# Kernel optimization log

Measured on AMD Instinct MI355X. Metric: run time of the kernel, lower is better.

Reference implementation:

```python
import jax, jax.numpy as jnp
import numpy as np

EMBED = 1024
HEADS = 16
HEAD_DIM = EMBED // HEADS
HIDDEN = 4096
EPS = 1e-5


def setup_inputs() -> dict:
    key = jax.random.key(0)
    ks = jax.random.split(key, 16)
    s_e = 1.0 / np.sqrt(EMBED)
    s_h = 1.0 / np.sqrt(HIDDEN)
    return {
        "x": jax.random.normal(ks[0], (8, 1024, EMBED), dtype=jnp.float32),
        "ln1_g": jnp.ones((EMBED,), jnp.float32),
        "ln1_b": jnp.zeros((EMBED,), jnp.float32),
        "ln2_g": jnp.ones((EMBED,), jnp.float32),
        "ln2_b": jnp.zeros((EMBED,), jnp.float32),
        "wq": jax.random.uniform(ks[1], (EMBED, EMBED), jnp.float32, -s_e, s_e),
        "bq": jax.random.uniform(ks[2], (EMBED,), jnp.float32, -s_e, s_e),
        "wk": jax.random.uniform(ks[3], (EMBED, EMBED), jnp.float32, -s_e, s_e),
        "bk": jax.random.uniform(ks[4], (EMBED,), jnp.float32, -s_e, s_e),
        "wv": jax.random.uniform(ks[5], (EMBED, EMBED), jnp.float32, -s_e, s_e),
        "bv": jax.random.uniform(ks[6], (EMBED,), jnp.float32, -s_e, s_e),
        "wo": jax.random.uniform(ks[7], (EMBED, EMBED), jnp.float32, -s_e, s_e),
        "bo": jax.random.uniform(ks[8], (EMBED,), jnp.float32, -s_e, s_e),
        "w1": jax.random.uniform(ks[9], (EMBED, HIDDEN), jnp.float32, -s_e, s_e),
        "b1": jax.random.uniform(ks[10], (HIDDEN,), jnp.float32, -s_e, s_e),
        "w2": jax.random.uniform(ks[11], (HIDDEN, EMBED), jnp.float32, -s_h, s_h),
        "b2": jax.random.uniform(ks[12], (EMBED,), jnp.float32, -s_h, s_h),
    }


def _layernorm(x, g, b):
    mu = jnp.mean(x, axis=-1, keepdims=True)
    var = jnp.mean((x - mu) ** 2, axis=-1, keepdims=True)
    return (x - mu) * jax.lax.rsqrt(var + EPS) * g + b


def reference(x, ln1_g, ln1_b, ln2_g, ln2_b, wq, bq, wk, bk, wv, bv, wo, bo, w1, b1, w2, b2):
    B, N, E = x.shape
    scale = HEAD_DIM ** (-0.5)
    # --- attention sublayer (pre-norm) ---
    h = _layernorm(x, ln1_g, ln1_b)
    q = (h @ wq + bq).reshape(B, N, HEADS, HEAD_DIM).transpose(0, 2, 1, 3) * scale
    k = (h @ wk + bk).reshape(B, N, HEADS, HEAD_DIM).transpose(0, 2, 1, 3)
    v = (h @ wv + bv).reshape(B, N, HEADS, HEAD_DIM).transpose(0, 2, 1, 3)
    scores = jnp.einsum("bhqd,bhkd->bhqk", q, k)
    attn = jax.nn.softmax(scores, axis=-1)
    ctx = jnp.einsum("bhqk,bhkd->bhqd", attn, v)
    ctx = ctx.transpose(0, 2, 1, 3).reshape(B, N, E)
    x = x + (ctx @ wo + bo)
    # --- FFN sublayer (pre-norm) ---
    h2 = _layernorm(x, ln2_g, ln2_b)
    ff = jax.nn.relu(h2 @ w1 + b1) @ w2 + b2
    return x + ff
```

## Files before the change

### kernel.cpp

```cpp
#include <hip/hip_runtime.h>
#include <hip/hip_bf16.h>

typedef __attribute__((ext_vector_type(4))) float f32x4;
typedef __attribute__((ext_vector_type(16))) float f32x16;
typedef __attribute__((ext_vector_type(8))) __bf16 bf16x8;
typedef __attribute__((ext_vector_type(4))) __bf16 bf16x4;
typedef __attribute__((ext_vector_type(4))) unsigned int u32x4;

static constexpr int E    = 1024;
static constexpr int TOK  = 8192;
static constexpr int HID  = 4096;

#define DEVINL __device__ __forceinline__

DEVINL void gload16(const void* g, void* l) {
  __builtin_amdgcn_global_load_lds((__attribute__((address_space(1))) void*)g,
                                   (__attribute__((address_space(3))) void*)l, 16, 0, 0);
}

#define ABAR()  asm volatile("s_barrier" ::: "memory")
#define AVM(n)  asm volatile("s_waitcnt vmcnt(" #n ")" ::: "memory")
#define CVTPK(dst, lo, hi) asm("v_cvt_pk_bf16_f32 %0, %1, %2" : "=v"(dst) : "v"(lo), "v"(hi))
#define PLSWAP(a, b) asm("v_permlane32_swap_b32 %0, %1" : "+v"(a), "+v"(b))

template <int N> DEVINL void avm() {
  if constexpr (N == 0)      asm volatile("s_waitcnt vmcnt(0)" ::: "memory");
  else if constexpr (N == 2) asm volatile("s_waitcnt vmcnt(2)" ::: "memory");
  else if constexpr (N == 8) asm volatile("s_waitcnt vmcnt(8)" ::: "memory");
  else if constexpr (N == 9) asm volatile("s_waitcnt vmcnt(9)" ::: "memory");
  else                       asm volatile("s_waitcnt vmcnt(0)" ::: "memory");
}

__global__ __launch_bounds__(256) void wconv_kernel(const float* __restrict__ W,
                                                    __bf16* __restrict__ Wt,
                                                    int K, int N) {
  __shared__ float tile[32][33];
  const int t  = threadIdx.x;
  const long k0 = (long)blockIdx.y * 32;
  const long n0 = (long)blockIdx.x * 32;
  const int r  = t >> 3;
  const int c4 = (t & 7) * 4;
  float4 v = *(const float4*)&W[(k0 + r) * N + n0 + c4];
  tile[r][c4 + 0] = v.x; tile[r][c4 + 1] = v.y;
  tile[r][c4 + 2] = v.z; tile[r][c4 + 3] = v.w;
  __syncthreads();
  bf16x4 o;
#pragma unroll
  for (int i = 0; i < 4; ++i) o[i] = (__bf16)tile[c4 + i][r];
  *(bf16x4*)&Wt[(n0 + r) * K + k0 + c4] = o;
}

__global__ __launch_bounds__(256) void ln_kernel(const float* __restrict__ X,
                                                 const float* __restrict__ g,
                                                 const float* __restrict__ be,
                                                 __bf16* __restrict__ O) {
  const int t = threadIdx.x;
  const long row = blockIdx.x;
  float4 v = *(const float4*)&X[row * E + t * 4];
  float s  = v.x + v.y + v.z + v.w;
  float ss = v.x * v.x + v.y * v.y + v.z * v.z + v.w * v.w;
#pragma unroll
  for (int off = 32; off; off >>= 1) {
    s  += __shfl_down(s, off);
    ss += __shfl_down(ss, off);
  }
  __shared__ float red[8];
  const int w = t >> 6;
  if ((t & 63) == 0) { red[w] = s; red[4 + w] = ss; }
  __syncthreads();
  s  = red[0] + red[1] + red[2] + red[3];
  ss = red[4] + red[5] + red[6] + red[7];
  const float mean = s * (1.0f / E);
  const float var  = ss * (1.0f / E) - mean * mean;
  const float rstd = rsqrtf(var + 1e-5f);
  float4 gv = *(const float4*)&g[t * 4];
  float4 bv = *(const float4*)&be[t * 4];
  bf16x4 o;
  o[0] = (__bf16)((v.x - mean) * rstd * gv.x + bv.x);
  o[1] = (__bf16)((v.y - mean) * rstd * gv.y + bv.y);
  o[2] = (__bf16)((v.z - mean) * rstd * gv.z + bv.z);
  o[3] = (__bf16)((v.w - mean) * rstd * gv.w + bv.w);
  *(bf16x4*)&O[row * E + t * 4] = o;
}

template <int BM_, int DEPTH, bool RELU, bool RESID, bool OUTBF, int NB>
__global__ __launch_bounds__(512, 2) void gemmk_kernel(const __bf16* __restrict__ A,
                                                       const __bf16* __restrict__ Bt,
                                                       const float* __restrict__ bias0,
                                                       const float* __restrict__ bias1,
                                                       const float* __restrict__ bias2,
                                                       const float* resid,
                                                       void* Cout,
                                                       int M, int N, int K) {
  extern __shared__ char lds[];
  constexpr int MF    = BM_ / 32;
  constexpr int ABYT  = BM_ * 64;
  constexpr int TILEB = ABYT + 16384;
  constexpr int AL    = BM_ / 128;
  constexpr int TL    = AL + 2;
  constexpr int W     = (DEPTH - 2) * TL;

  const int tid  = threadIdx.x;
  const int lane = tid & 63;
  const int l15  = lane & 15;
  const int kp   = lane >> 4;
  const int wid  = tid >> 6;
  const int wr   = wid >> 2;
  const int wc   = wid & 3;

  const int nwg  = gridDim.x * gridDim.y;
  const int flat = blockIdx.x + gridDim.x * blockIdx.y;
  const int swz  = (flat & 7) * (nwg >> 3) + (flat >> 3);
  const int bx   = swz % gridDim.x;
  const int by   = swz / gridDim.x;
  const long brow = (long)by * BM_;
  const long bcol = (long)bx * 256;

  const __bf16* Ab = A  + brow * K;
  const __bf16* Bb = Bt + bcol * K;
  const int NT = K >> 5;

  auto stageA = [&](int k0, char* dst) {
#pragma unroll
    for (int i = 0; i < AL; ++i) {
      const int c = i * 512 + tid;
      const int r = c >> 2;
      const int p = (c & 3) ^ ((r >> 1) & 3);
      gload16(Ab + (long)r * K + k0 + p * 8, dst + c * 16);
    }
  };
  auto stageB = [&](int k0, char* dst) {
#pragma unroll
    for (int i = 0; i < 2; ++i) {
      const int c = i * 512 + tid;
      const int r = c >> 2;
      const int p = (c & 3) ^ ((r >> 1) & 3);
      gload16(Bb + (long)r * K + k0 + p * 8, dst + c * 16);
    }
  };

  f32x4 acc[MF][4];
  const f32x4 z4 = {0.f, 0.f, 0.f, 0.f};
#pragma unroll
  for (int m = 0; m < MF; ++m)
#pragma unroll
    for (int n = 0; n < 4; ++n) acc[m][n] = z4;

#pragma unroll
  for (int pt = 0; pt < DEPTH - 1; ++pt) {
    stageA(pt * 32, lds + pt * TILEB);
    stageB(pt * 32, lds + pt * TILEB + ABYT);
  }

  bf16x8 af[MF > 4 ? 4 : MF], bfr[4];

  for (int t = 0; t < NT; ++t) {
    const int cb = t % DEPTH;
    const int sb = (t + DEPTH - 1) % DEPTH;
    const char* Ac = lds + cb * TILEB;
    const char* Bc = Ac + ABYT;
    char* An = lds + sb * TILEB;
    const int kt = (t + DEPTH - 1 < NT) ? ((t + DEPTH - 1) << 5) : 0;

    avm<W>();
    ABAR();

    if constexpr (BM_ == 256) {
#pragma unroll
      for (int m = 0; m < 4; ++m) {
        const int row = m * 32 + wr * 16 + l15;
        af[m] = *(const bf16x8*)(Ac + row * 64 + (kp ^ ((row >> 1) & 3)) * 16);
      }
#pragma unroll
      for (int n = 0; n < 4; ++n) {
        const int col = n * 64 + wc * 16 + l15;
        bfr[n] = *(const bf16x8*)(Bc + col * 64 + (kp ^ ((col >> 1) & 3)) * 16);
      }
      stageA(kt, An);
      __builtin_amdgcn_s_setprio(1);
#pragma unroll
      for (int m = 0; m < 4; ++m)
#pragma unroll
        for (int n = 0; n < 4; ++n)
          acc[m][n] = __builtin_amdgcn_mfma_f32_16x16x32_bf16(af[m], bfr[n], acc[m][n], 0, 0, 0);
      __builtin_amdgcn_s_setprio(0);
#pragma unroll
      for (int m = 0; m < 4; ++m) {
        const int row = (m + 4) * 32 + wr * 16 + l15;
        af[m] = *(const bf16x8*)(Ac + row * 64 + (kp ^ ((row >> 1) & 3)) * 16);
      }
      stageB(kt, An + ABYT);
      __builtin_amdgcn_s_setprio(1);
#pragma unroll
      for (int m = 0; m < 4; ++m)
#pragma unroll
        for (int n = 0; n < 4; ++n)
          acc[m + 4][n] = __builtin_amdgcn_mfma_f32_16x16x32_bf16(af[m], bfr[n], acc[m + 4][n], 0, 0, 0);
      __builtin_amdgcn_s_setprio(0);
    } else {
#pragma unroll
      for (int m = 0; m < 4; ++m) {
        const int row = m * 32 + wr * 16 + l15;
        af[m] = *(const bf16x8*)(Ac + row * 64 + (kp ^ ((row >> 1) & 3)) * 16);
      }
#pragma unroll
      for (int n = 0; n < 4; ++n) {
        const int col = n * 64 + wc * 16 + l15;
        bfr[n] = *(const bf16x8*)(Bc + col * 64 + (kp ^ ((col >> 1) & 3)) * 16);
      }
      stageA(kt, An);
      stageB(kt, An + ABYT);
      __builtin_amdgcn_s_setprio(1);
#pragma unroll
      for (int m = 0; m < 4; ++m)
#pragma unroll
        for (int n = 0; n < 4; ++n)
          acc[m][n] = __builtin_amdgcn_mfma_f32_16x16x32_bf16(af[m], bfr[n], acc[m][n], 0, 0, 0);
      __builtin_amdgcn_s_setprio(0);
    }
  }
  avm<0>();

#pragma unroll
  for (int m = 0; m < MF; ++m) {
#pragma unroll
    for (int n = 0; n < 4; ++n) {
      const long col = bcol + n * 64 + wc * 16 + l15;
      float bb;
      if (NB == 3) {
        const float* bp = (col < 1024) ? bias0 : ((col < 2048) ? bias1 : bias2);
        bb = bp[col & 1023];
      } else {
        bb = bias0[col];
      }
#pragma unroll
      for (int j = 0; j < 4; ++j) {
        const long row = brow + m * 32 + wr * 16 + (lane >> 4) * 4 + j;
        float val = acc[m][n][j] + bb;
        if (RELU) val = fmaxf(val, 0.f);
        const long idx = row * N + col;
        if (RESID) val += resid[idx];
        if (OUTBF) ((__bf16*)Cout)[idx] = (__bf16)val;
        else       ((float*)Cout)[idx]  = val;
      }
    }
  }
}

__global__ __launch_bounds__(256, 3) void attn_kernel(const __bf16* __restrict__ QKV,
                                                      __bf16* __restrict__ Og) {
  __shared__ __align__(16) __bf16 Qs[128 * 64];
  __shared__ __align__(16) __bf16 Ks[2][64 * 64];
  __shared__ __align__(16) __bf16 Vt[2][64 * 64];

  const int QSTR = 3072;
  const int t    = threadIdx.x;
  const int lane = t & 63;
  const int w    = t >> 6;
  const int l31  = lane & 31;
  const int h    = lane >> 5;
  const int b    = blockIdx.y >> 4;
  const int hh   = blockIdx.y & 15;
  const long row0 = (long)b * 1024 + (long)blockIdx.x * 128;
  const long kvrow0 = (long)b * 1024;
  const int colQ = hh * 64;
  const int colK = colQ + 1024;
  const int colV = colQ + 2048;

#pragma unroll
  for (int j = 0; j < 4; ++j) {
    const int c = j * 256 + t;
    const int r = c >> 3;
    const int p = (c & 7) ^ (r & 7);
    gload16(QKV + (row0 + r) * QSTR + colQ + p * 8, (char*)Qs + c * 16);
  }
#pragma unroll
  for (int j = 0; j < 2; ++j) {
    const int c = j * 256 + t;
    const int r = c >> 3;
    const int p = (c & 7) ^ (r & 7);
    gload16(QKV + (kvrow0 + r) * QSTR + colK + p * 8, (char*)Ks[0] + c * 16);
  }
  bf16x8 vv[2];
#pragma unroll
  for (int j = 0; j < 2; ++j) {
    const int c = j * 256 + t;
    const int key = c >> 3, dc = c & 7;
    vv[j] = *(const bf16x8*)(QKV + (kvrow0 + key) * QSTR + colV + dc * 8);
  }
  AVM(0);
#pragma unroll
  for (int j = 0; j < 2; ++j) {
    const int c = j * 256 + t;
    const int key = c >> 3, dc = c & 7;
#pragma unroll
    for (int e = 0; e < 8; ++e) {
      const int d = dc * 8 + e;
      *(__bf16*)((char*)Vt[0] + d * 128 + (((key >> 3) ^ dc) * 16) + (key & 7) * 2) = vv[j][e];
    }
  }
  __syncthreads();

  bf16x8 bq[4];
  {
    const int qrow = w * 32 + l31;
#pragma unroll
    for (int kk = 0; kk < 4; ++kk) {
      const int p = (kk * 2 + h) ^ (qrow & 7);
      bq[kk] = *(const bf16x8*)((const char*)Qs + qrow * 128 + p * 16);
    }
  }

  f32x16 ctx0, ctx1;
#pragma unroll
  for (int r = 0; r < 16; ++r) { ctx0[r] = 0.f; ctx1[r] = 0.f; }
  float m = -INFINITY, l = 0.f;

  for (int kb = 0; kb < 16; ++kb) {
    const int cur = kb & 1, nxt = cur ^ 1;
    const int kb1 = (kb + 1 < 16) ? kb + 1 : kb;
    const long kr1 = kvrow0 + kb1 * 64;

#pragma unroll
    for (int j = 0; j < 2; ++j) {
      const int c = j * 256 + t;
      const int key = c >> 3, dc = c & 7;
      vv[j] = *(const bf16x8*)(QKV + (kr1 + key) * QSTR + colV + dc * 8);
    }
#pragma unroll
    for (int j = 0; j < 2; ++j) {
      const int c = j * 256 + t;
      const int r = c >> 3;
      const int p = (c & 7) ^ (r & 7);
      gload16(QKV + (kr1 + r) * QSTR + colK + p * 8, (char*)Ks[nxt] + c * 16);
    }

    f32x16 s0, s1;
#pragma unroll
    for (int r = 0; r < 16; ++r) { s0[r] = 0.f; s1[r] = 0.f; }
    __builtin_amdgcn_s_setprio(1);
#pragma unroll
    for (int kk = 0; kk < 4; ++kk) {
      const int pce = kk * 2 + h;
      const int p0i = pce ^ (l31 & 7);
      bf16x8 ak0 = *(const bf16x8*)((const char*)Ks[cur] + l31 * 128 + p0i * 16);
      bf16x8 ak1 = *(const bf16x8*)((const char*)Ks[cur] + (32 + l31) * 128 + p0i * 16);
      s0 = __builtin_amdgcn_mfma_f32_32x32x16_bf16(ak0, bq[kk], s0, 0, 0, 0);
      s1 = __builtin_amdgcn_mfma_f32_32x32x16_bf16(ak1, bq[kk], s1, 0, 0, 0);
    }
    __builtin_amdgcn_s_setprio(0);

    float mx = s0[0];
#pragma unroll
    for (int r = 1; r < 16; ++r) mx = fmaxf(mx, s0[r]);
#pragma unroll
    for (int r = 0; r < 16; ++r) mx = fmaxf(mx, s1[r]);
    mx = fmaxf(mx, __shfl_xor(mx, 32));

    if (!__all(mx - m <= 64.f)) {
      const float mn = fmaxf(m, mx);
      const float corr = __expf((m - mn) * 0.125f);
      l *= corr;
#pragma unroll
      for (int r = 0; r < 16; ++r) { ctx0[r] *= corr; ctx1[r] *= corr; }
      m = mn;
    }
    f32x16 p0, p1;
    float rs = 0.f;
#pragma unroll
    for (int r = 0; r < 16; ++r) { p0[r] = __expf((s0[r] - m) * 0.125f); rs += p0[r]; }
#pragma unroll
    for (int r = 0; r < 16; ++r) { p1[r] = __expf((s1[r] - m) * 0.125f); rs += p1[r]; }
    rs += __shfl_xor(rs, 32);
    l += rs;

    AVM(2);
#pragma unroll
    for (int j = 0; j < 2; ++j) {
      const int c = j * 256 + t;
      const int key = c >> 3, dc = c & 7;
#pragma unroll
      for (int e = 0; e < 8; ++e) {
        const int d = dc * 8 + e;
        *(__bf16*)((char*)Vt[nxt] + d * 128 + (((key >> 3) ^ dc) * 16) + (key & 7) * 2) = vv[j][e];
      }
    }

    bf16x8 paf[4];
#pragma unroll
    for (int ks = 0; ks < 4; ++ks) {
      const int base = (ks & 1) * 8;
      unsigned a0, a1, b0, b1;
      if (ks < 2) {
        CVTPK(a0, p0[base + 0], p0[base + 1]);
        CVTPK(b0, p0[base + 4], p0[base + 5]);
        CVTPK(a1, p0[base + 2], p0[base + 3]);
        CVTPK(b1, p0[base + 6], p0[base + 7]);
      } else {
        CVTPK(a0, p1[base + 0], p1[base + 1]);
        CVTPK(b0, p1[base + 4], p1[base + 5]);
        CVTPK(a1, p1[base + 2], p1[base + 3]);
        CVTPK(b1, p1[base + 6], p1[base + 7]);
      }
      PLSWAP(a0, b0);
      PLSWAP(a1, b1);
      u32x4 wv4; wv4[0] = a0; wv4[1] = a1; wv4[2] = b0; wv4[3] = b1;
      paf[ks] = __builtin_bit_cast(bf16x8, wv4);
    }

    __builtin_amdgcn_s_setprio(1);
#pragma unroll
    for (int ks = 0; ks < 4; ++ks) {
      const int pce = ks * 2 + h;
      bf16x8 av0 = *(const bf16x8*)((const char*)Vt[cur] + l31 * 128 + ((pce ^ (l31 >> 3)) * 16));
      bf16x8 av1 = *(const bf16x8*)((const char*)Vt[cur] + (32 + l31) * 128 + ((pce ^ (4 + (l31 >> 3))) * 16));
      ctx0 = __builtin_amdgcn_mfma_f32_32x32x16_bf16(av0, paf[ks], ctx0, 0, 0, 0);
      ctx1 = __builtin_amdgcn_mfma_f32_32x32x16_bf16(av1, paf[ks], ctx1, 0, 0, 0);
    }
    __builtin_amdgcn_s_setprio(0);

    __syncthreads();
  }

  const float inv = 1.0f / l;
  const long orow = row0 + w * 32 + l31;
#pragma unroll
  for (int f = 0; f < 2; ++f)
#pragma unroll
    for (int tq = 0; tq < 4; ++tq) {
      bf16x4 o;
#pragma unroll
      for (int e = 0; e < 4; ++e) {
        const float v = (f ? ctx1[tq * 4 + e] : ctx0[tq * 4 + e]) * inv;
        o[e] = (__bf16)v;
      }
      const int col = colQ + f * 32 + tq * 8 + h * 4;
      *(bf16x4*)&Og[orow * E + col] = o;
    }
}

extern "C" void kernel_launch(void* const* d_in, const int* in_sizes, int n_in,
                              void* d_out, int out_size, void* d_ws, size_t ws_size,
                              hipStream_t stream) {
  const float* x     = (const float*)d_in[0];
  const float* ln1g  = (const float*)d_in[1];
  const float* ln1b  = (const float*)d_in[2];
  const float* ln2g  = (const float*)d_in[3];
  const float* ln2b  = (const float*)d_in[4];
  const float* wq    = (const float*)d_in[5];
  const float* bq    = (const float*)d_in[6];
  const float* wk    = (const float*)d_in[7];
  const float* bk    = (const float*)d_in[8];
  const float* wv    = (const float*)d_in[9];
  const float* bv    = (const float*)d_in[10];
  const float* wo    = (const float*)d_in[11];
  const float* bo    = (const float*)d_in[12];
  const float* w1    = (const float*)d_in[13];
  const float* b1    = (const float*)d_in[14];
  const float* w2    = (const float*)d_in[15];
  const float* b2    = (const float*)d_in[16];
  float* out = (float*)d_out;

  char* ws = (char*)d_ws;
  const size_t MB = 1024 * 1024;
  __bf16* Wqkv = (__bf16*)(ws + 0 * MB);
  __bf16* Wot  = (__bf16*)(ws + 6 * MB);
  __bf16* W1t  = (__bf16*)(ws + 8 * MB);
  __bf16* W2t  = (__bf16*)(ws + 16 * MB);
  __bf16* h    = (__bf16*)(ws + 24 * MB);
  __bf16* qkv  = (__bf16*)(ws + 40 * MB);
  __bf16* ctx  = (__bf16*)(ws + 88 * MB);
  __bf16* ff1  = (__bf16*)(ws + 40 * MB);

  const dim3 blk(256);
  const dim3 blk512(512);
  const size_t GLDS256 = 4 * (256 * 64 + 16384);
  const size_t GLDS128 = 5 * (128 * 64 + 16384);

  wconv_kernel<<<dim3(E / 32, E / 32), blk, 0, stream>>>(wq, Wqkv, E, E);
  wconv_kernel<<<dim3(E / 32, E / 32), blk, 0, stream>>>(wk, Wqkv + 1024 * 1024, E, E);
  wconv_kernel<<<dim3(E / 32, E / 32), blk, 0, stream>>>(wv, Wqkv + 2048 * 1024, E, E);
  wconv_kernel<<<dim3(E / 32, E / 32), blk, 0, stream>>>(wo, Wot, E, E);
  wconv_kernel<<<dim3(HID / 32, E / 32), blk, 0, stream>>>(w1, W1t, E, HID);
  wconv_kernel<<<dim3(E / 32, HID / 32), blk, 0, stream>>>(w2, W2t, HID, E);

  ln_kernel<<<TOK, blk, 0, stream>>>(x, ln1g, ln1b, h);

  gemmk_kernel<256, 4, false, false, true, 3><<<dim3(3072 / 256, TOK / 256), blk512, GLDS256, stream>>>(
      h, Wqkv, bq, bk, bv, nullptr, qkv, TOK, 3072, E);

  attn_kernel<<<dim3(8, 128), blk, 0, stream>>>(qkv, ctx);

  gemmk_kernel<128, 5, false, true, false, 1><<<dim3(E / 256, TOK / 128), blk512, GLDS128, stream>>>(
      ctx, Wot, bo, nullptr, nullptr, x, out, TOK, E, E);

  ln_kernel<<<TOK, blk, 0, stream>>>(out, ln2g, ln2b, h);

  gemmk_kernel<256, 4, true, false, true, 1><<<dim3(HID / 256, TOK / 256), blk512, GLDS256, stream>>>(
      h, W1t, b1, nullptr, nullptr, nullptr, ff1, TOK, HID, E);

  gemmk_kernel<128, 5, false, true, false, 1><<<dim3(E / 256, TOK / 128), blk512, GLDS128, stream>>>(
      ff1, W2t, b2, nullptr, nullptr, out, out, TOK, E, HID);
}
```

Baseline: 367.1 us.

## Split-K the FFN down-projection into two bf16 partials plus a reduce kernel

The W2 GEMM (K=4096) now runs as a 2-way split-K with 256-row tiles, writing bf16 partial sums to two scratch buffers. A new reduce kernel then adds the partials, the bias and the residual into the output. The GEMM main loop also gains extra barriers and lgkmcnt(0) waits with sched_barrier around the MFMA blocks, pinning the instruction schedule. The trade is more wave-level parallelism and bigger tiles against extra global traffic, bf16 rounding of the partial sums, and added synchronisation in every GEMM.

Measured after the change: 364.8 us. About the same (-0.6%).

```diff
diff --git a/kernel.cpp b/kernel.cpp
--- a/kernel.cpp
+++ b/kernel.cpp
@@ -20,6 +20,8 @@
 
 #define ABAR()  asm volatile("s_barrier" ::: "memory")
 #define AVM(n)  asm volatile("s_waitcnt vmcnt(" #n ")" ::: "memory")
+#define ALGKM0() do { asm volatile("s_waitcnt lgkmcnt(0)" ::: "memory"); \
+                      __builtin_amdgcn_sched_barrier(0); } while (0)
 #define CVTPK(dst, lo, hi) asm("v_cvt_pk_bf16_f32 %0, %1, %2" : "=v"(dst) : "v"(lo), "v"(hi))
 #define PLSWAP(a, b) asm("v_permlane32_swap_b32 %0, %1" : "+v"(a), "+v"(b))
 
@@ -83,6 +85,22 @@
   *(bf16x4*)&O[row * E + t * 4] = o;
 }
 
+__global__ __launch_bounds__(256) void reduce2_kernel(float* __restrict__ out,
+                                                      const __bf16* __restrict__ t0,
+                                                      const __bf16* __restrict__ t1,
+                                                      const float* __restrict__ b2) {
+  const int i = blockIdx.x * 256 + threadIdx.x;
+  float4 o = ((const float4*)out)[i];
+  bf16x4 a = ((const bf16x4*)t0)[i];
+  bf16x4 b = ((const bf16x4*)t1)[i];
+  float4 bb = ((const float4*)b2)[i & 255];
+  o.x += bb.x + (float)a[0] + (float)b[0];
+  o.y += bb.y + (float)a[1] + (float)b[1];
+  o.z += bb.z + (float)a[2] + (float)b[2];
+  o.w += bb.w + (float)a[3] + (float)b[3];
+  ((float4*)out)[i] = o;
+}
+
 template <int BM_, int DEPTH, bool RELU, bool RESID, bool OUTBF, int NB>
 __global__ __launch_bounds__(512, 2) void gemmk_kernel(const __bf16* __restrict__ A,
                                                        const __bf16* __restrict__ Bt,
@@ -90,8 +108,8 @@
                                                        const float* __restrict__ bias1,
                                                        const float* __restrict__ bias2,
                                                        const float* resid,
-                                                       void* Cout,
-                                                       int M, int N, int K) {
+                                                       void* Cout, void* Cout2,
+                                                       int M, int N, int K, int KLD) {
   extern __shared__ char lds[];
   constexpr int MF    = BM_ / 32;
   constexpr int ABYT  = BM_ * 64;
@@ -108,16 +126,20 @@
   const int wr   = wid >> 2;
   const int wc   = wid & 3;
 
-  const int nwg  = gridDim.x * gridDim.y;
-  const int flat = blockIdx.x + gridDim.x * blockIdx.y;
+  const int gx   = gridDim.x, gy = gridDim.y;
+  const int nwg  = gx * gy * gridDim.z;
+  const int flat = blockIdx.x + gx * (blockIdx.y + gy * blockIdx.z);
   const int swz  = (flat & 7) * (nwg >> 3) + (flat >> 3);
-  const int bx   = swz % gridDim.x;
-  const int by   = swz / gridDim.x;
+  const int bx   = swz % gx;
+  const int by   = (swz / gx) % gy;
+  const int bz   = swz / (gx * gy);
   const long brow = (long)by * BM_;
   const long bcol = (long)bx * 256;
-
-  const __bf16* Ab = A  + brow * K;
-  const __bf16* Bb = Bt + bcol * K;
+  const long koff = (long)bz * K;
+
+  const __bf16* Ab = A  + brow * KLD + koff;
+  const __bf16* Bb = Bt + bcol * KLD + koff;
+  void* Cdst = bz ? Cout2 : Cout;
   const int NT = K >> 5;
 
   auto stageA = [&](int k0, char* dst) {
@@ -126,7 +148,7 @@
       const int c = i * 512 + tid;
       const int r = c >> 2;
       const int p = (c & 3) ^ ((r >> 1) & 3);
-      gload16(Ab + (long)r * K + k0 + p * 8, dst + c * 16);
+      gload16(Ab + (long)r * KLD + k0 + p * 8, dst + c * 16);
     }
   };
   auto stageB = [&](int k0, char* dst) {
@@ -135,7 +157,7 @@
       const int c = i * 512 + tid;
       const int r = c >> 2;
       const int p = (c & 3) ^ ((r >> 1) & 3);
-      gload16(Bb + (long)r * K + k0 + p * 8, dst + c * 16);
+      gload16(Bb + (long)r * KLD + k0 + p * 8, dst + c * 16);
     }
   };
 
@@ -152,7 +174,7 @@
     stageB(pt * 32, lds + pt * TILEB + ABYT);
   }
 
-  bf16x8 af[MF > 4 ? 4 : MF], bfr[4];
+  bf16x8 af[4], bfr[4];
 
   for (int t = 0; t < NT; ++t) {
     const int cb = t % DEPTH;
@@ -177,6 +199,8 @@
         bfr[n] = *(const bf16x8*)(Bc + col * 64 + (kp ^ ((col >> 1) & 3)) * 16);
       }
       stageA(kt, An);
+      ABAR();
+      ALGKM0();
       __builtin_amdgcn_s_setprio(1);
 #pragma unroll
       for (int m = 0; m < 4; ++m)
@@ -184,12 +208,15 @@
         for (int n = 0; n < 4; ++n)
           acc[m][n] = __builtin_amdgcn_mfma_f32_16x16x32_bf16(af[m], bfr[n], acc[m][n], 0, 0, 0);
       __builtin_amdgcn_s_setprio(0);
+      ABAR();
 #pragma unroll
       for (int m = 0; m < 4; ++m) {
         const int row = (m + 4) * 32 + wr * 16 + l15;
         af[m] = *(const bf16x8*)(Ac + row * 64 + (kp ^ ((row >> 1) & 3)) * 16);
       }
       stageB(kt, An + ABYT);
+      ABAR();
+      ALGKM0();
       __builtin_amdgcn_s_setprio(1);
 #pragma unroll
       for (int m = 0; m < 4; ++m)
@@ -210,6 +237,8 @@
       }
       stageA(kt, An);
       stageB(kt, An + ABYT);
+      ABAR();
+      ALGKM0();
       __builtin_amdgcn_s_setprio(1);
 #pragma unroll
       for (int m = 0; m < 4; ++m)
@@ -230,8 +259,10 @@
       if (NB == 3) {
         const float* bp = (col < 1024) ? bias0 : ((col < 2048) ? bias1 : bias2);
         bb = bp[col & 1023];
+      } else if (NB == 1) {
+        bb = bias0[col];
       } else {
-        bb = bias0[col];
+        bb = 0.f;
       }
 #pragma unroll
       for (int j = 0; j < 4; ++j) {
@@ -240,8 +271,8 @@
         if (RELU) val = fmaxf(val, 0.f);
         const long idx = row * N + col;
         if (RESID) val += resid[idx];
-        if (OUTBF) ((__bf16*)Cout)[idx] = (__bf16)val;
-        else       ((float*)Cout)[idx]  = val;
+        if (OUTBF) ((__bf16*)Cdst)[idx] = (__bf16)val;
+        else       ((float*)Cdst)[idx]  = val;
       }
     }
   }
@@ -471,6 +502,8 @@
   __bf16* qkv  = (__bf16*)(ws + 40 * MB);
   __bf16* ctx  = (__bf16*)(ws + 88 * MB);
   __bf16* ff1  = (__bf16*)(ws + 40 * MB);
+  __bf16* tmp0 = (__bf16*)(ws + 0 * MB);
+  __bf16* tmp1 = (__bf16*)(ws + 24 * MB);
 
   const dim3 blk(256);
   const dim3 blk512(512);
@@ -487,18 +520,20 @@
   ln_kernel<<<TOK, blk, 0, stream>>>(x, ln1g, ln1b, h);
 
   gemmk_kernel<256, 4, false, false, true, 3><<<dim3(3072 / 256, TOK / 256), blk512, GLDS256, stream>>>(
-      h, Wqkv, bq, bk, bv, nullptr, qkv, TOK, 3072, E);
+      h, Wqkv, bq, bk, bv, nullptr, qkv, nullptr, TOK, 3072, E, E);
 
   attn_kernel<<<dim3(8, 128), blk, 0, stream>>>(qkv, ctx);
 
   gemmk_kernel<128, 5, false, true, false, 1><<<dim3(E / 256, TOK / 128), blk512, GLDS128, stream>>>(
-      ctx, Wot, bo, nullptr, nullptr, x, out, TOK, E, E);
+      ctx, Wot, bo, nullptr, nullptr, x, out, nullptr, TOK, E, E, E);
 
   ln_kernel<<<TOK, blk, 0, stream>>>(out, ln2g, ln2b, h);
 
   gemmk_kernel<256, 4, true, false, true, 1><<<dim3(HID / 256, TOK / 256), blk512, GLDS256, stream>>>(
-      h, W1t, b1, nullptr, nullptr, nullptr, ff1, TOK, HID, E);
-
-  gemmk_kernel<128, 5, false, true, false, 1><<<dim3(E / 256, TOK / 128), blk512, GLDS128, stream>>>(
-      ff1, W2t, b2, nullptr, nullptr, out, out, TOK, E, HID);
-}
+      h, W1t, b1, nullptr, nullptr, nullptr, ff1, nullptr, TOK, HID, E, E);
+
+  gemmk_kernel<256, 4, false, false, true, 0><<<dim3(E / 256, TOK / 256, 2), blk512, GLDS256, stream>>>(
+      ff1, W2t, nullptr, nullptr, nullptr, nullptr, tmp0, tmp1, TOK, E, HID / 2, HID);
+
+  reduce2_kernel<<<TOK * E / 1024, blk, 0, stream>>>(out, tmp0, tmp1, b2);
+}
```
